# Kernel tuning notes

Hardware: AMD Instinct MI355X
Metric: run time of the kernel (lower is better)

## Reference

```python
import jax, jax.numpy as jnp
import numpy as np

HEADS = 4
OUT_CH = 16
NEG_SLOPE = 0.2


def setup_inputs() -> dict:
    key = jax.random.key(0)
    k1, k2, k3, k4 = jax.random.split(key, 4)
    N, E, IN = 50000, 800000, 128
    x = jax.random.normal(k1, (N, IN), dtype=jnp.float32)
    edge_index = jax.random.randint(k2, (2, E), 0, N, dtype=jnp.int32)
    weight = jax.random.normal(k3, (IN, HEADS * OUT_CH), dtype=jnp.float32) * 0.1
    att = jax.random.normal(k4, (1, HEADS, 2 * OUT_CH), dtype=jnp.float32) * 0.1
    bias = jnp.zeros((HEADS * OUT_CH,), dtype=jnp.float32)
    return {"x": x, "edge_index": edge_index, "weight": weight, "att": att, "bias": bias}


def reference(x, edge_index, weight, att, bias):
    N = x.shape[0]
    # add self loops
    loops = jnp.broadcast_to(jnp.arange(N, dtype=edge_index.dtype)[None, :], (2, N))
    ei = jnp.concatenate([edge_index, loops], axis=1)  # [2, E+N]
    h = (x @ weight).reshape(N, HEADS, OUT_CH)  # [N, H, C]
    row, col = ei[0], ei[1]
    x_i = h[row]  # [E', H, C]
    x_j = h[col]  # [E', H, C]
    att_i = att[:, :, :OUT_CH]  # [1, H, C]
    att_j = att[:, :, OUT_CH:]
    alpha = (x_i * att_i).sum(-1) + (x_j * att_j).sum(-1)  # [E', H]
    alpha = jax.nn.leaky_relu(alpha, NEG_SLOPE)
    # NOTE: faithful to the source, softmax over the heads dim (dim=1)
    alpha = jax.nn.softmax(alpha, axis=1)
    out = jnp.zeros((N, HEADS, OUT_CH), dtype=x.dtype)
    out = out.at[col].add(x_i * alpha[..., None])  # scatter-add over destination col
    out = out.reshape(N, HEADS * OUT_CH) + bias
    return out
```

## Files before the change

kernel.cpp:

```cpp
#include <hip/hip_runtime.h>

#define HEADS 4
#define OUT_CH 16
#define CCH 64
#define IN_CH 128
#define NEG_SLOPE 0.2f
#define CAP 48
#define CAPB 5120
#define TILE_A 2048

typedef unsigned int       uint32;
typedef unsigned long long u64;
typedef unsigned short     u16;
typedef __attribute__((ext_vector_type(8))) short short8;
typedef __attribute__((ext_vector_type(4))) float f32x4;

__device__ __forceinline__ uint32 bf16_rne(float f) {
    uint32 u = __float_as_uint(f);
    return (u + 0x7fffu + ((u >> 16) & 1u)) >> 16;
}

__global__ __launch_bounds__(256) void k_pre(int* __restrict__ cur, int N,
                                             const float* __restrict__ x,
                                             const float* __restrict__ w,
                                             const float* __restrict__ att,
                                             u16* __restrict__ wTg,
                                             int* __restrict__ bcur, int NBUK,
                                             float* __restrict__ d_i,
                                             float* __restrict__ d_j,
                                             int ZB) {
    int t = threadIdx.x;
    int b = blockIdx.x;

    if (b < ZB) {
        int i = b * 256 + t;
        if (i < N) cur[i] = 0;
        return;
    }
    if (b == ZB) {
        int c = t & 63, half = t >> 6;
        #pragma unroll
        for (int kk = 0; kk < 32; ++kk) {
            int k = half * 32 + kk;
            wTg[c * 128 + k] = (u16)bf16_rne(w[k * CCH + c]);
        }
        if (t < NBUK) bcur[t] = 0;
        return;
    }

    __shared__ float wXf[8][132];
    for (int idx = t; idx < 1024; idx += 256) {
        int k = idx >> 3, j = idx & 7, h = j & 3;
        const float* ab = att + h * (2 * OUT_CH) + ((j >= 4) ? OUT_CH : 0);
        float s = 0.f;
        #pragma unroll
        for (int c = 0; c < 16; ++c)
            s = fmaf(w[k * CCH + h * OUT_CH + c], ab[c], s);
        wXf[j][k] = s;
    }
    __syncthreads();

    int r = (b - ZB - 1) * 32 + (t >> 3);
    int j = t & 7;
    if (r >= N) return;
    const float4* x4 = (const float4*)(x + (size_t)r * IN_CH);
    float s0 = 0.f, s1 = 0.f, s2 = 0.f, s3 = 0.f;
    #pragma unroll
    for (int k4 = 0; k4 < 32; ++k4) {
        float4 v = x4[k4];
        s0 = fmaf(v.x, wXf[j][k4 * 4 + 0], s0);
        s1 = fmaf(v.y, wXf[j][k4 * 4 + 1], s1);
        s2 = fmaf(v.z, wXf[j][k4 * 4 + 2], s2);
        s3 = fmaf(v.w, wXf[j][k4 * 4 + 3], s3);
    }
    float d = (s0 + s1) + (s2 + s3);
    if (j < 4) d_i[r * HEADS + j] = d;
    else       d_j[r * HEADS + (j - 4)] = d;
}

__global__ __launch_bounds__(256) void k_fat(const float* __restrict__ x,
                                             const u16* __restrict__ wTg,
                                             u16* __restrict__ h_bf,
                                             const int* __restrict__ rows,
                                             const int* __restrict__ cols,
                                             const float* __restrict__ d_i,
                                             const float* __restrict__ d_j,
                                             int* __restrict__ bcur,
                                             uint4* __restrict__ bucketbuf,
                                             int N, int E, int GB, int NBUK) {
    int t = threadIdx.x;

    if ((int)blockIdx.x < GB) {
        int lane = t & 63;
        int col = lane & 15, g = (lane >> 4) * 8;
        int tile = blockIdx.x * 4 + (t >> 6);
        int ntiles = (N + 15) >> 4;
        if (tile >= ntiles) return;

        int r0 = tile * 16 + (lane & 15);
        if (r0 >= N) r0 = N - 1;
        const float* xp = x + (size_t)r0 * IN_CH + g;
        float4 cu[8];
        #pragma unroll
        for (int kc = 0; kc < 4; ++kc) {
            cu[kc * 2]     = *(const float4*)(xp + kc * 32);
            cu[kc * 2 + 1] = *(const float4*)(xp + kc * 32 + 4);
        }

        short8 bfrag[4][4];
        #pragma unroll
        for (int nt = 0; nt < 4; ++nt)
            #pragma unroll
            for (int kc = 0; kc < 4; ++kc)
                bfrag[nt][kc] = *(const short8*)&wTg[(nt * 16 + col) * 128 + kc * 32 + g];

        short8 af[4];
        #pragma unroll
        for (int kc = 0; kc < 4; ++kc) {
            float4 u = cu[kc * 2], v = cu[kc * 2 + 1];
            short8 s;
            s[0] = (short)bf16_rne(u.x); s[1] = (short)bf16_rne(u.y);
            s[2] = (short)bf16_rne(u.z); s[3] = (short)bf16_rne(u.w);
            s[4] = (short)bf16_rne(v.x); s[5] = (short)bf16_rne(v.y);
            s[6] = (short)bf16_rne(v.z); s[7] = (short)bf16_rne(v.w);
            af[kc] = s;
        }

        f32x4 acc[4] = {{0.f,0.f,0.f,0.f},{0.f,0.f,0.f,0.f},
                        {0.f,0.f,0.f,0.f},{0.f,0.f,0.f,0.f}};
        #pragma unroll
        for (int kc = 0; kc < 4; ++kc)
            #pragma unroll
            for (int nt = 0; nt < 4; ++nt)
                acc[nt] = __builtin_amdgcn_mfma_f32_16x16x32_bf16(
                    af[kc], bfrag[nt][kc], acc[nt], 0, 0, 0);

        int rb = tile * 16;
        #pragma unroll
        for (int nt = 0; nt < 4; ++nt)
            #pragma unroll
            for (int r = 0; r < 4; ++r) {
                int row = rb + (lane >> 4) * 4 + r;
                if (row < N)
                    h_bf[(size_t)row * CCH + nt * 16 + col] =
                        (u16)bf16_rne(acc[nt][r]);
            }
    } else {
        __shared__ int lcnt[256];
        __shared__ int lbase[256];
        int b = (int)blockIdx.x - GB;
        int e0 = b * TILE_A;
        int tot = E + N;

        lcnt[t] = 0;
        __syncthreads();

        int mybkt[8], myrank[8];
        #pragma unroll
        for (int i = 0; i < 8; ++i) {
            int e = e0 + i * 256 + t;
            if (e < tot) {
                int c = (e < E) ? cols[e] : (e - E);
                int bk = c >> 8;
                mybkt[i] = bk;
                myrank[i] = atomicAdd(&lcnt[bk], 1);
            } else {
                mybkt[i] = -1;
            }
        }
        __syncthreads();
        if (t < NBUK && lcnt[t] > 0) lbase[t] = atomicAdd(&bcur[t], lcnt[t]);
        __syncthreads();

        #pragma unroll
        for (int i = 0; i < 8; ++i) {
            if (mybkt[i] < 0) continue;
            int e = e0 + i * 256 + t;
            int r, c;
            if (e < E) { r = rows[e]; c = cols[e]; }
            else       { r = e - E;   c = r; }

            float4 di4 = *(const float4*)(d_i + (size_t)r * HEADS);
            float4 dj4 = *(const float4*)(d_j + (size_t)c * HEADS);
            float l0 = di4.x + dj4.x, l1 = di4.y + dj4.y;
            float l2 = di4.z + dj4.z, l3 = di4.w + dj4.w;
            l0 = l0 > 0.f ? l0 : NEG_SLOPE * l0;
            l1 = l1 > 0.f ? l1 : NEG_SLOPE * l1;
            l2 = l2 > 0.f ? l2 : NEG_SLOPE * l2;
            l3 = l3 > 0.f ? l3 : NEG_SLOPE * l3;
            float m = fmaxf(fmaxf(l0, l1), fmaxf(l2, l3));
            float e0f = __expf(l0 - m), e1f = __expf(l1 - m);
            float e2f = __expf(l2 - m), e3f = __expf(l3 - m);
            float inv = 1.f / (e0f + e1f + e2f + e3f);

            uint32 q0 = (uint32)(e0f * inv * 2047.f + 0.5f);
            uint32 q1 = (uint32)(e1f * inv * 2047.f + 0.5f);
            uint32 q2 = (uint32)(e2f * inv * 2047.f + 0.5f);
            uint32 q3 = (uint32)(e3f * inv * 2047.f + 0.5f);

            int gpos = lbase[mybkt[i]] + myrank[i];
            if (gpos < CAPB)
                bucketbuf[(size_t)mybkt[i] * CAPB + gpos] =
                    make_uint4((uint32)r, (uint32)c,
                               q0 | (q1 << 11), q2 | (q3 << 11));
        }
    }
}

__global__ __launch_bounds__(256) void k_bucket(const int* __restrict__ bcur,
                                                const uint4* __restrict__ bucketbuf,
                                                u64* __restrict__ srec,
                                                int* __restrict__ cur, int N) {
    __shared__ u64 win[256 * CAP];
    __shared__ int lcur[256];
    int t = threadIdx.x;
    int b = blockIdx.x;

    lcur[t] = 0;
    __syncthreads();

    int cnt = bcur[b];
    if (cnt > CAPB) cnt = CAPB;
    const uint4* bb = bucketbuf + (size_t)b * CAPB;
    for (int i = t; i < cnt; i += 256) {
        uint4 rec = bb[i];
        int crel = rec.y & 255;
        int pos = atomicAdd(&lcur[crel], 1);
        if (pos < CAP)
            win[crel * CAP + pos] =
                (u64)rec.x | ((u64)rec.z << 17) | ((u64)rec.w << 39);
    }
    __syncthreads();

    int c0 = b << 8;
    int nd = N - c0;
    if (nd > 256) nd = 256;
    int nent = nd * CAP;
    u64* dst = srec + (size_t)c0 * CAP;
    for (int i = t; i < nent; i += 256) dst[i] = win[i];
    if (t < nd) {
        int v = lcur[t];
        cur[c0 + t] = (v > CAP) ? CAP : v;
    }
}

__global__ __launch_bounds__(256) void k_accum(const int* __restrict__ cur,
                                               const u64* __restrict__ srec,
                                               const u16* __restrict__ h_bf,
                                               const float* __restrict__ bias,
                                               float* __restrict__ out, int N) {
    int t = threadIdx.x;
    int wid = t >> 6, lane = t & 63;
    int g = lane >> 4, sub = lane & 15;
    int node = blockIdx.x * 16 + wid * 4 + g;
    int c = (node < N) ? node : N - 1;

    int dg = cur[c];
    if (dg > CAP) dg = CAP;
    int s = c * CAP;
    int md = dg;
    md = max(md, __shfl_xor(md, 16));
    md = max(md, __shfl_xor(md, 32));

    int shift = 17 + 11 * (sub >> 2);
    float a0 = 0.f, a1 = 0.f, a2 = 0.f, a3 = 0.f;

    #pragma unroll 8
    for (int r = 0; r < md; ++r) {
        int idx = s + ((r < dg) ? r : (dg - 1));
        u64 rec = srec[idx];
        int row = (int)((uint32)rec & 0x1FFFFu);
        float a = (float)((uint32)(rec >> shift) & 0x7FFu) * (1.f / 2047.f);
        if (r >= dg) a = 0.f;
        uint2 hb = *(const uint2*)(h_bf + (size_t)row * CCH + sub * 4);
        a0 = fmaf(__uint_as_float(hb.x << 16),         a, a0);
        a1 = fmaf(__uint_as_float(hb.x & 0xffff0000u), a, a1);
        a2 = fmaf(__uint_as_float(hb.y << 16),         a, a2);
        a3 = fmaf(__uint_as_float(hb.y & 0xffff0000u), a, a3);
    }

    if (node < N) {
        float4 b = *(const float4*)(bias + sub * 4);
        float4 o = {a0 + b.x, a1 + b.y, a2 + b.z, a3 + b.w};
        *(float4*)(out + (size_t)node * CCH + sub * 4) = o;
    }
}

extern "C" void kernel_launch(void* const* d_in, const int* in_sizes, int n_in,
                              void* d_out, int out_size, void* d_ws, size_t ws_size,
                              hipStream_t stream) {
    const float* x    = (const float*)d_in[0];
    const int*   ei   = (const int*)  d_in[1];
    const float* w    = (const float*)d_in[2];
    const float* att  = (const float*)d_in[3];
    const float* bias = (const float*)d_in[4];
    float* out = (float*)d_out;

    int N = in_sizes[0] / IN_CH;
    int E = in_sizes[1] / 2;
    const int* rows = ei;
    const int* cols = ei + E;
    int total_e = E + N;
    int NBUK = (N + 255) >> 8;

    char* ws = (char*)d_ws;
    auto carve = [&](size_t bytes) {
        char* p = ws;
        ws += (bytes + 255) & ~(size_t)255;
        return p;
    };
    u16*   h_bf      = (u16*)  carve((size_t)N * CCH * 2);
    float* di        = (float*)carve((size_t)N * HEADS * 4);
    float* dj        = (float*)carve((size_t)N * HEADS * 4);
    int*   cur       = (int*)  carve((size_t)N * 4);
    int*   bcur      = (int*)  carve((size_t)NBUK * 4);
    u64*   srec      = (u64*)  carve((size_t)N * CAP * 8);
    u16*   wTg       = (u16*)  carve((size_t)64 * 128 * 2);
    uint4* bucketbuf = (uint4*)carve((size_t)NBUK * CAPB * 16);

    int ntiles = (N + 15) >> 4;
    int GB = (ntiles + 3) / 4;
    int AB = (total_e + TILE_A - 1) / TILE_A;
    int ZB = (N + 255) / 256;
    int DB = (N + 31) / 32;

    k_pre<<<ZB + 1 + DB, 256, 0, stream>>>(cur, N, x, w, att, wTg, bcur, NBUK,
                                           di, dj, ZB);
    k_fat<<<GB + AB, 256, 0, stream>>>(x, wTg, h_bf, rows, cols, di, dj,
                                       bcur, bucketbuf, N, E, GB, NBUK);
    k_bucket<<<NBUK, 256, 0, stream>>>(bcur, bucketbuf, srec, cur, N);
    k_accum<<<(N + 15) / 16, 256, 0, stream>>>(cur, srec, h_bf, bias, out, N);
}
```

Baseline: 97.55 us.

## Move softmax into accumulation and shrink edge records to packed 32-bit

The per-edge leaky-relu/softmax moves out of the bucketing pass into k_accum, which gathers d_i per source row and uses the destination's d_j directly. Edge records shrink from 16-byte bucket entries and 8-byte sorted records to a single packed 32-bit word (row plus local column). Bucketing stages records in shared memory via a prefix scan so global writes are coalesced, and bucket counters are padded to avoid atomic contention on shared cache lines. This cuts bucket and record traffic and replaces 11-bit quantized weights with full-precision ones. The cost is an extra d_i gather and recomputed exponentials per edge in the accumulation loop.

```diff
diff --git a/kernel.cpp b/kernel.cpp
--- a/kernel.cpp
+++ b/kernel.cpp
@@ -8,9 +8,9 @@
 #define CAP 48
 #define CAPB 5120
 #define TILE_A 2048
+#define BSTRIDE 32
 
 typedef unsigned int       uint32;
-typedef unsigned long long u64;
 typedef unsigned short     u16;
 typedef __attribute__((ext_vector_type(8))) short short8;
 typedef __attribute__((ext_vector_type(4))) float f32x4;
@@ -44,7 +44,7 @@
             int k = half * 32 + kk;
             wTg[c * 128 + k] = (u16)bf16_rne(w[k * CCH + c]);
         }
-        if (t < NBUK) bcur[t] = 0;
+        for (int i = t; i < NBUK * BSTRIDE; i += 256) bcur[i] = 0;
         return;
     }
 
@@ -83,10 +83,8 @@
                                              u16* __restrict__ h_bf,
                                              const int* __restrict__ rows,
                                              const int* __restrict__ cols,
-                                             const float* __restrict__ d_i,
-                                             const float* __restrict__ d_j,
                                              int* __restrict__ bcur,
-                                             uint4* __restrict__ bucketbuf,
+                                             uint32* __restrict__ bucketbuf,
                                              int N, int E, int GB, int NBUK) {
     int t = threadIdx.x;
 
@@ -147,71 +145,78 @@
             }
     } else {
         __shared__ int lcnt[256];
+        __shared__ int lofs[256];
         __shared__ int lbase[256];
+        __shared__ int wsum[4];
+        __shared__ uint32 recbuf[TILE_A];
+        __shared__ int    gbuf[TILE_A];
         int b = (int)blockIdx.x - GB;
         int e0 = b * TILE_A;
         int tot = E + N;
+        int lane = t & 63, wid = t >> 6;
 
         lcnt[t] = 0;
         __syncthreads();
 
         int mybkt[8], myrank[8];
+        uint32 myrec[8];
         #pragma unroll
         for (int i = 0; i < 8; ++i) {
             int e = e0 + i * 256 + t;
             if (e < tot) {
                 int c = (e < E) ? cols[e] : (e - E);
+                int r = (e < E) ? rows[e] : c;
                 int bk = c >> 8;
                 mybkt[i] = bk;
+                myrec[i] = (uint32)r | ((uint32)(c & 255) << 17);
                 myrank[i] = atomicAdd(&lcnt[bk], 1);
             } else {
                 mybkt[i] = -1;
             }
         }
         __syncthreads();
-        if (t < NBUK && lcnt[t] > 0) lbase[t] = atomicAdd(&bcur[t], lcnt[t]);
+
+        int v = lcnt[t];
+        int sc = v;
+        #pragma unroll
+        for (int off = 1; off < 64; off <<= 1) {
+            int u = __shfl_up(sc, off);
+            if (lane >= off) sc += u;
+        }
+        if (lane == 63) wsum[wid] = sc;
+        __syncthreads();
+        int wb = 0;
+        for (int j = 0; j < wid; ++j) wb += wsum[j];
+        lofs[t] = wb + sc - v;
+        if (t < NBUK && v > 0)
+            lbase[t] = atomicAdd(&bcur[t * BSTRIDE], v);
         __syncthreads();
 
         #pragma unroll
         for (int i = 0; i < 8; ++i) {
             if (mybkt[i] < 0) continue;
-            int e = e0 + i * 256 + t;
-            int r, c;
-            if (e < E) { r = rows[e]; c = cols[e]; }
-            else       { r = e - E;   c = r; }
-
-            float4 di4 = *(const float4*)(d_i + (size_t)r * HEADS);
-            float4 dj4 = *(const float4*)(d_j + (size_t)c * HEADS);
-            float l0 = di4.x + dj4.x, l1 = di4.y + dj4.y;
-            float l2 = di4.z + dj4.z, l3 = di4.w + dj4.w;
-            l0 = l0 > 0.f ? l0 : NEG_SLOPE * l0;
-            l1 = l1 > 0.f ? l1 : NEG_SLOPE * l1;
-            l2 = l2 > 0.f ? l2 : NEG_SLOPE * l2;
-            l3 = l3 > 0.f ? l3 : NEG_SLOPE * l3;
-            float m = fmaxf(fmaxf(l0, l1), fmaxf(l2, l3));
-            float e0f = __expf(l0 - m), e1f = __expf(l1 - m);
-            float e2f = __expf(l2 - m), e3f = __expf(l3 - m);
-            float inv = 1.f / (e0f + e1f + e2f + e3f);
-
-            uint32 q0 = (uint32)(e0f * inv * 2047.f + 0.5f);
-            uint32 q1 = (uint32)(e1f * inv * 2047.f + 0.5f);
-            uint32 q2 = (uint32)(e2f * inv * 2047.f + 0.5f);
-            uint32 q3 = (uint32)(e3f * inv * 2047.f + 0.5f);
-
-            int gpos = lbase[mybkt[i]] + myrank[i];
-            if (gpos < CAPB)
-                bucketbuf[(size_t)mybkt[i] * CAPB + gpos] =
-                    make_uint4((uint32)r, (uint32)c,
-                               q0 | (q1 << 11), q2 | (q3 << 11));
+            int bk = mybkt[i];
+            int slot = lofs[bk] + myrank[i];
+            int bpos = lbase[bk] + myrank[i];
+            recbuf[slot] = myrec[i];
+            gbuf[slot] = (bpos < CAPB) ? (bk * CAPB + bpos) : -1;
+        }
+        __syncthreads();
+
+        int nrec = tot - e0;
+        if (nrec > TILE_A) nrec = TILE_A;
+        for (int sidx = t; sidx < nrec; sidx += 256) {
+            int gp = gbuf[sidx];
+            if (gp >= 0) bucketbuf[gp] = recbuf[sidx];
         }
     }
 }
 
 __global__ __launch_bounds__(256) void k_bucket(const int* __restrict__ bcur,
-                                                const uint4* __restrict__ bucketbuf,
-                                                u64* __restrict__ srec,
+                                                const uint32* __restrict__ bucketbuf,
+                                                uint32* __restrict__ srec,
                                                 int* __restrict__ cur, int N) {
-    __shared__ u64 win[256 * CAP];
+    __shared__ uint32 win[256 * CAP];
     __shared__ int lcur[256];
     int t = threadIdx.x;
     int b = blockIdx.x;
@@ -219,16 +224,15 @@
     lcur[t] = 0;
     __syncthreads();
 
-    int cnt = bcur[b];
+    int cnt = bcur[b * BSTRIDE];
     if (cnt > CAPB) cnt = CAPB;
-    const uint4* bb = bucketbuf + (size_t)b * CAPB;
+    const uint32* bb = bucketbuf + (size_t)b * CAPB;
     for (int i = t; i < cnt; i += 256) {
-        uint4 rec = bb[i];
-        int crel = rec.y & 255;
+        uint32 rec = bb[i];
+        int crel = (rec >> 17) & 255;
         int pos = atomicAdd(&lcur[crel], 1);
         if (pos < CAP)
-            win[crel * CAP + pos] =
-                (u64)rec.x | ((u64)rec.z << 17) | ((u64)rec.w << 39);
+            win[crel * CAP + pos] = rec & 0x1FFFFu;
     }
     __syncthreads();
 
@@ -236,7 +240,7 @@
     int nd = N - c0;
     if (nd > 256) nd = 256;
     int nent = nd * CAP;
-    u64* dst = srec + (size_t)c0 * CAP;
+    uint32* dst = srec + (size_t)c0 * CAP;
     for (int i = t; i < nent; i += 256) dst[i] = win[i];
     if (t < nd) {
         int v = lcur[t];
@@ -245,8 +249,10 @@
 }
 
 __global__ __launch_bounds__(256) void k_accum(const int* __restrict__ cur,
-                                               const u64* __restrict__ srec,
+                                               const uint32* __restrict__ srec,
                                                const u16* __restrict__ h_bf,
+                                               const float* __restrict__ d_i,
+                                               const float* __restrict__ d_j,
                                                const float* __restrict__ bias,
                                                float* __restrict__ out, int N) {
     int t = threadIdx.x;
@@ -262,21 +268,33 @@
     md = max(md, __shfl_xor(md, 16));
     md = max(md, __shfl_xor(md, 32));
 
-    int shift = 17 + 11 * (sub >> 2);
+    float4 dj4 = *(const float4*)(d_j + (size_t)c * HEADS);
+    int hsel = sub >> 2;
     float a0 = 0.f, a1 = 0.f, a2 = 0.f, a3 = 0.f;
 
-    #pragma unroll 8
+    #pragma unroll 4
     for (int r = 0; r < md; ++r) {
         int idx = s + ((r < dg) ? r : (dg - 1));
-        u64 rec = srec[idx];
-        int row = (int)((uint32)rec & 0x1FFFFu);
-        float a = (float)((uint32)(rec >> shift) & 0x7FFu) * (1.f / 2047.f);
+        int row = (int)srec[idx];
+        float4 di4 = *(const float4*)(d_i + (size_t)row * HEADS);
+        float l0 = di4.x + dj4.x, l1 = di4.y + dj4.y;
+        float l2 = di4.z + dj4.z, l3 = di4.w + dj4.w;
+        l0 = l0 > 0.f ? l0 : NEG_SLOPE * l0;
+        l1 = l1 > 0.f ? l1 : NEG_SLOPE * l1;
+        l2 = l2 > 0.f ? l2 : NEG_SLOPE * l2;
+        l3 = l3 > 0.f ? l3 : NEG_SLOPE * l3;
+        float m = fmaxf(fmaxf(l0, l1), fmaxf(l2, l3));
+        float e0 = __expf(l0 - m), e1 = __expf(l1 - m);
+        float e2 = __expf(l2 - m), e3 = __expf(l3 - m);
+        float inv = 1.f / (e0 + e1 + e2 + e3);
+        float eh = (hsel < 2) ? (hsel == 0 ? e0 : e1) : (hsel == 2 ? e2 : e3);
+        float a = eh * inv;
         if (r >= dg) a = 0.f;
         uint2 hb = *(const uint2*)(h_bf + (size_t)row * CCH + sub * 4);
-        a0 = fmaf(__uint_as_float(hb.x << 16),         a, a0);
-        a1 = fmaf(__uint_as_float(hb.x & 0xffff0000u), a, a1);
-        a2 = fmaf(__uint_as_float(hb.y << 16),         a, a2);
-        a3 = fmaf(__uint_as_float(hb.y & 0xffff0000u), a, a3);
+        a0 = fmaf(__uint_as_float(hb.x << 16),           a, a0);
+        a1 = fmaf(__uint_as_float(hb.x & 0xffff0000u),   a, a1);
+        a2 = fmaf(__uint_as_float(hb.y << 16),           a, a2);
+        a3 = fmaf(__uint_as_float(hb.y & 0xffff0000u),   a, a3);
     }
 
     if (node < N) {
@@ -309,14 +327,14 @@
         ws += (bytes + 255) & ~(size_t)255;
         return p;
     };
-    u16*   h_bf      = (u16*)  carve((size_t)N * CCH * 2);
-    float* di        = (float*)carve((size_t)N * HEADS * 4);
-    float* dj        = (float*)carve((size_t)N * HEADS * 4);
-    int*   cur       = (int*)  carve((size_t)N * 4);
-    int*   bcur      = (int*)  carve((size_t)NBUK * 4);
-    u64*   srec      = (u64*)  carve((size_t)N * CAP * 8);
-    u16*   wTg       = (u16*)  carve((size_t)64 * 128 * 2);
-    uint4* bucketbuf = (uint4*)carve((size_t)NBUK * CAPB * 16);
+    u16*    h_bf      = (u16*)   carve((size_t)N * CCH * 2);
+    float*  di        = (float*) carve((size_t)N * HEADS * 4);
+    float*  dj        = (float*) carve((size_t)N * HEADS * 4);
+    int*    cur       = (int*)   carve((size_t)N * 4);
+    int*    bcur      = (int*)   carve((size_t)NBUK * BSTRIDE * 4);
+    uint32* srec      = (uint32*)carve((size_t)N * CAP * 4);
+    u16*    wTg       = (u16*)   carve((size_t)64 * 128 * 2);
+    uint32* bucketbuf = (uint32*)carve((size_t)NBUK * CAPB * 4);
 
     int ntiles = (N + 15) >> 4;
     int GB = (ntiles + 3) / 4;
@@ -326,8 +344,8 @@
 
     k_pre<<<ZB + 1 + DB, 256, 0, stream>>>(cur, N, x, w, att, wTg, bcur, NBUK,
                                            di, dj, ZB);
-    k_fat<<<GB + AB, 256, 0, stream>>>(x, wTg, h_bf, rows, cols, di, dj,
+    k_fat<<<GB + AB, 256, 0, stream>>>(x, wTg, h_bf, rows, cols,
                                        bcur, bucketbuf, N, E, GB, NBUK);
     k_bucket<<<NBUK, 256, 0, stream>>>(bcur, bucketbuf, srec, cur, N);
-    k_accum<<<(N + 15) / 16, 256, 0, stream>>>(cur, srec, h_bf, bias, out, N);
-}
+    k_accum<<<(N + 15) / 16, 256, 0, stream>>>(cur, srec, h_bf, di, dj, bias, out, N);
+}
```

New measurement: 97.97 us. No clear change (+0.4%).
